# Kernel optimization log

Measured on AMD Instinct MI355X. Metric: run time of the kernel, lower is better.

## Reference

```python
import jax, jax.numpy as jnp
import numpy as np

C = 12        # num_cls
KN = 5        # kernel_num
MU = 2        # kernel_mu
N = 384       # ns == nt (prob_mtx assumes equal sizes)
D = 256       # feature dim


def _cdist(a, b):
    # Euclidean pairwise distance (torch.cdist, p=2)
    d2 = (jnp.sum(a * a, 1)[:, None] + jnp.sum(b * b, 1)[None, :]
          - 2.0 * (a @ b.T))
    return jnp.sqrt(jnp.maximum(d2, 0.0))


def _kern(dist, gamma):
    # dist: (..., N, N) broadcastable against gamma (...,)
    # multi-bandwidth RBF: sum_i exp(-clip(dist / max(gamma*mu^(i-kn//2), 1e-5), 1e-5, 1e5))
    g = gamma[..., None, None]
    acc = 0.0
    for i in range(KN):
        bw = jnp.maximum(g * (MU ** (i - KN // 2)), 1e-5)
        r = jnp.clip(dist / bw, 1e-5, 1e5)
        acc = acc + jnp.exp(-r)
    return acc


def setup_inputs() -> dict:
    key = jax.random.key(0)
    k1, k2, k3, k4 = jax.random.split(key, 4)
    src_x = jax.random.normal(k1, (N, D), dtype=jnp.float32)
    tgt_x = jax.random.normal(k2, (N, D), dtype=jnp.float32)
    src_y = jax.random.randint(k3, (N,), 0, C)
    t = jax.random.uniform(k4, (N, C), dtype=jnp.float32) + 1e-3
    tgt_y = t / t.sum(axis=1, keepdims=True)  # soft pseudo-label probs
    return {"src_x": src_x, "tgt_x": tgt_x, "src_y": src_y, "tgt_y": tgt_y}


def _cdd(src_x, tgt_x, ps, pt):
    E_ss = _cdist(src_x, src_x)
    E_tt = _cdist(tgt_x, tgt_x)
    E_st = _cdist(src_x, tgt_x)

    # per-class weighted distance sums: sum_ij p_i p_j E_ij
    sss = jnp.einsum('ic,ij,jc->c', ps, E_ss, ps)
    stt = jnp.einsum('ic,ij,jc->c', pt, E_tt, pt)
    sst = jnp.einsum('is,ij,jt->st', ps, E_st, pt)
    cs = ps.sum(0)
    ct = pt.sum(0)
    pss = cs * cs          # (C,)  == prob['ss'][c].sum()
    ptt = ct * ct
    pst = cs[:, None] * ct[None, :]  # (C,C)

    # ---------------- intra (diagonal class pairs, src vs tgt) ----------------
    g_in = jax.lax.stop_gradient(
        (sss + stt + 2.0 * jnp.diagonal(sst))
        / (pss + ptt + 2.0 * jnp.diagonal(pst)))   # (C,)

    Pss = ps.T[:, :, None] * ps.T[:, None, :]      # (C,N,N)
    Ptt = pt.T[:, :, None] * pt.T[:, None, :]      # (C,N,N)
    Pst = ps.T[:, :, None] * pt.T[:, None, :]      # (C,N,N) diagonal pairs

    Dss = E_ss[None] * Pss
    Dtt = E_tt[None] * Ptt
    Dst = E_st[None] * Pst

    k1 = (_kern(Dss, g_in) * Pss).sum((-2, -1)) / pss
    k2 = (_kern(Dtt, g_in) * Ptt).sum((-2, -1)) / ptt
    k3 = (_kern(Dst, g_in) * Pst).sum((-2, -1)) / jnp.diagonal(pst)
    intra = (k1 + k2 - 2.0 * k3).sum() / C

    # ---------------- inter (off-diagonal class pairs, src only) --------------
    # edist['ss']==edist['tt']==edist['st']==E_ss; probs from (src_y, src_y)
    sst_s = jnp.einsum('is,ij,jt->st', ps, E_ss, ps)       # (C,C)
    pst_s = cs[:, None] * cs[None, :]
    g2 = jax.lax.stop_gradient(
        (sss[:, None] + sss[None, :] + 2.0 * sst_s)
        / (pss[:, None] + pss[None, :] + 2.0 * pst_s))     # (C,C)

    K1 = _kern(Dss[:, None], g2)                            # (C,C,N,N)
    T1 = jnp.einsum('stij,sij->st', K1, Pss) / pss[:, None]
    K2 = _kern(Dss[None, :], g2)
    T2 = jnp.einsum('stij,tij->st', K2, Pss) / pss[None, :]
    Pst2 = ps.T[:, None, :, None] * ps.T[None, :, None, :]  # (C,C,N,N)
    K3 = _kern(E_ss[None, None] * Pst2, g2)
    T3 = (K3 * Pst2).sum((-2, -1)) / pst_s

    mmd = (T1 + T2 - 2.0 * T3) * (1.0 - jnp.eye(C, dtype=T1.dtype))
    inter = mmd.sum() / (C * C - C)
    return intra, inter


def reference(src_x, tgt_x, src_y, tgt_y):
    ps = jnp.eye(C, dtype=src_x.dtype)[src_y]  # one-hot like torch.eye(num_cls)[src_y]
    return _cdd(src_x, tgt_x, ps, tgt_y)
```

## Files before the change

### kernel.cpp

```cpp
#include <hip/hip_runtime.h>
#include <math.h>

#define NN 147456
#define Nn 384
#define Dd 256
#define Cc 12
#define NTILE 144

__device__ __forceinline__ float kern5(float d, const float* __restrict__ ibw) {
    float acc = 0.f;
#pragma unroll
    for (int k = 0; k < 5; k++) {
        float r = fminf(fmaxf(d * ibw[k], 1e-5f), 1e5f);
        acc += __expf(-r);
    }
    return acc;
}

__device__ __forceinline__ float blockReduceSum(float v, float* sh) {
#pragma unroll
    for (int o = 32; o; o >>= 1) v += __shfl_xor(v, o, 64);
    __syncthreads();
    if ((threadIdx.x & 63) == 0) sh[threadIdx.x >> 6] = v;
    __syncthreads();
    float r = 0.f;
    if (threadIdx.x == 0) {
        int nw = (int)(blockDim.x >> 6);
        for (int w = 0; w < nw; w++) r += sh[w];
    }
    return r;
}

__global__ __launch_bounds__(256) void cdist_stats_kernel(
        const float* __restrict__ sx, const float* __restrict__ tx,
        const int* __restrict__ ys, const float* __restrict__ pt,
        float* __restrict__ Ebase, float* __restrict__ P0T,
        float* __restrict__ P1T, float* __restrict__ P2T,
        float* __restrict__ out) {
    int z = blockIdx.z;
    int tid = threadIdx.x;
    int i0 = blockIdx.y * 32, j0 = blockIdx.x * 32;
    int tileIdx = blockIdx.y * 12 + blockIdx.x;
    if (z == 0 && tileIdx == 0 && tid < 2) out[tid] = 0.f;

    const float* X = (z == 1) ? tx : sx;
    const float* Y = (z == 0) ? sx : tx;
    float* Eo = Ebase + z * NN;

    __shared__ float As[32][33];
    __shared__ float Bs[32][33];
    __shared__ float red[144];
    __shared__ int   ysh[32];
    __shared__ float ptish[384];
    if (tid < 32) ysh[tid] = ys[i0 + tid];
    if (tid < 144) red[tid] = 0.f;
    if (z == 1)
        for (int q = tid; q < 384; q += 256) ptish[q] = pt[i0 * 12 + q];

    int tj = tid & 31, ti = tid >> 5;
    float acc[4] = {0.f, 0.f, 0.f, 0.f};
    for (int kk = 0; kk < Dd; kk += 32) {
#pragma unroll
        for (int p = 0; p < 4; p++) {
            int idx = tid + p * 256;
            int r = idx >> 5, k = idx & 31;
            As[r][k] = X[(i0 + r) * Dd + kk + k];
            Bs[r][k] = Y[(j0 + r) * Dd + kk + k];
        }
        __syncthreads();
#pragma unroll
        for (int m = 0; m < 4; m++) {
            int r = ti + m * 8;
            float a = 0.f;
#pragma unroll
            for (int k = 0; k < 32; k++) {
                float d = As[r][k] - Bs[tj][k];
                a = fmaf(d, d, a);
            }
            acc[m] += a;
        }
        __syncthreads();
    }
    float e[4];
#pragma unroll
    for (int m = 0; m < 4; m++) {
        e[m] = sqrtf(acc[m]);
        Eo[(i0 + ti + m * 8) * Nn + j0 + tj] = e[m];
    }

    if (z == 0) {
        int t = ys[j0 + tj];
#pragma unroll
        for (int m = 0; m < 4; m++)
            atomicAdd(&red[ysh[ti + m * 8] * 12 + t], e[m]);
        __syncthreads();
        if (tid < 144) P0T[tid * NTILE + tileIdx] = red[tid];
    } else {
        const float4* p4 = (const float4*)(pt + (j0 + tj) * 12);
        float4 pa = p4[0], pb = p4[1], pc = p4[2];
        float pv[12] = {pa.x, pa.y, pa.z, pa.w, pb.x, pb.y, pb.z, pb.w,
                        pc.x, pc.y, pc.z, pc.w};
#pragma unroll
        for (int c = 0; c < 12; c++) {
            float a = 0.f;
            if (z == 1) {
#pragma unroll
                for (int m = 0; m < 4; m++)
                    a = fmaf(e[m], ptish[(ti + m * 8) * 12 + c], a);
            } else {
#pragma unroll
                for (int m = 0; m < 4; m++)
                    a += (ysh[ti + m * 8] == c) ? e[m] : 0.f;
            }
            float v = a * pv[c];
#pragma unroll
            for (int o = 32; o; o >>= 1) v += __shfl_xor(v, o, 64);
            if ((tid & 63) == 0) atomicAdd(&red[c], v);
        }
        __syncthreads();
        if (tid < 12) {
            if (z == 1) P1T[tid * NTILE + tileIdx] = red[tid];
            else        P2T[tid * NTILE + tileIdx] = red[tid];
        }
    }
}

__global__ __launch_bounds__(384) void eval_kernel(
        const float* __restrict__ E, const int* __restrict__ ys,
        const float* __restrict__ pt, const float* __restrict__ P0T,
        const float* __restrict__ P1T, const float* __restrict__ P2T,
        float* __restrict__ out) {
    int i = blockIdx.x;
    int j = threadIdx.x;
    int s = ys[i];
    __shared__ float st48[48];
    __shared__ float s_cs[12], s_ct[12];
    __shared__ float sh_ibwin[60];
    __shared__ float sh_ibw2s[60];
    __shared__ float sh_invptt[12];
    __shared__ float sh_invccs[12];
    __shared__ float sh_pti[12];
    __shared__ float red[8];
    if (j >= 64 && j < 76)       s_cs[j - 64] = 0.f;
    else if (j >= 80 && j < 92)  s_ct[j - 80] = 0.f;
    else if (j >= 96 && j < 108) sh_pti[j - 96] = pt[i * 12 + (j - 96)];

    int t = ys[j];
    const float4* p4 = (const float4*)(pt + j * 12);
    float4 pa = p4[0], pb = p4[1], pc = p4[2];
    float ptj[12] = {pa.x, pa.y, pa.z, pa.w, pb.x, pb.y, pb.z, pb.w,
                     pc.x, pc.y, pc.z, pc.w};
    float e_ss = E[i * Nn + j];
    float e_tt = E[NN + i * Nn + j];
    float e_st = E[2 * NN + i * Nn + j];
    __syncthreads();

    atomicAdd(&s_cs[t], 1.f);
#pragma unroll
    for (int c = 0; c < 12; c++) {
        float v = ptj[c];
#pragma unroll
        for (int o = 32; o; o >>= 1) v += __shfl_xor(v, o, 64);
        if ((j & 63) == 0) atomicAdd(&s_ct[c], v);
    }
    {
        int g = j >> 3, k = j & 7;
        const float* src;
        if (g < 12)      src = P0T + (g * 13) * NTILE;
        else if (g < 24) src = P0T + (s * 12 + (g - 12)) * NTILE;
        else if (g < 36) src = P1T + (g - 24) * NTILE;
        else             src = P2T + (g - 36) * NTILE;
        float v = 0.f;
#pragma unroll
        for (int q = 0; q < 18; q++) v += src[k * 18 + q];
#pragma unroll
        for (int o = 1; o < 8; o <<= 1) v += __shfl_xor(v, o, 64);
        if (k == 0) st48[g] = v;
    }
    __syncthreads();
    const float MUP[5] = {0.25f, 0.5f, 1.f, 2.f, 4.f};
    if (j < 12) {
        int c = j;
        float cs = s_cs[c], ct2 = s_ct[c];
        float g = (st48[c] + st48[24 + c] + 2.f * st48[36 + c])
                  / ((cs + ct2) * (cs + ct2));
#pragma unroll
        for (int k = 0; k < 5; k++)
            sh_ibwin[c * 5 + k] = 1.f / fmaxf(g * MUP[k], 1e-5f);
        sh_invptt[c] = 1.f / (ct2 * ct2);
    } else if (j >= 64 && j < 76) {
        int tp = j - 64;
        float css = s_cs[s], cst = s_cs[tp];
        float g2 = (st48[s] + st48[tp] + 2.f * st48[12 + tp])
                   / ((css + cst) * (css + cst));
#pragma unroll
        for (int k = 0; k < 5; k++)
            sh_ibw2s[tp * 5 + k] = 1.f / fmaxf(g2 * MUP[k], 1e-5f);
        sh_invccs[tp] = 1.f / (css * cst);
    }
    __syncthreads();
    float invpss_s = 1.f / (s_cs[s] * s_cs[s]);
    float invcst_s = 1.f / (s_cs[s] * s_ct[s]);

    float si = 0.f, se = 0.f;
#pragma unroll
    for (int c = 0; c < 12; c++) {
        float w = sh_pti[c] * ptj[c];
        si = fmaf(kern5(e_tt * w, &sh_ibwin[c * 5]) * w, sh_invptt[c], si);
    }
    {
        float w = 0.f;
#pragma unroll
        for (int c = 0; c < 12; c++) w = (c == s) ? ptj[c] : w;
        si = fmaf(-2.f * kern5(e_st * w, &sh_ibwin[s * 5]) * w, invcst_s, si);
    }
    if (t == s) {
        si = fmaf(kern5(e_ss, &sh_ibwin[s * 5]), invpss_s, si);
        float ts = -kern5(e_ss, &sh_ibw2s[s * 5]);
#pragma unroll
        for (int tp = 0; tp < 12; tp++)
            ts += kern5(e_ss, &sh_ibw2s[tp * 5]);
        se = fmaf(2.f * ts, invpss_s, se);
    } else {
        se = fmaf(-2.f * kern5(e_ss, &sh_ibw2s[t * 5]), sh_invccs[t], se);
    }
    si = blockReduceSum(si, red);
    se = blockReduceSum(se, red);
    if (j == 0) {
        atomicAdd(&out[0], si * (1.f / 12.f));
        atomicAdd(&out[1], se * (1.f / 132.f));
    }
}

extern "C" void kernel_launch(void* const* d_in, const int* in_sizes, int n_in,
                              void* d_out, int out_size, void* d_ws, size_t ws_size,
                              hipStream_t stream) {
    (void)in_sizes; (void)n_in; (void)out_size; (void)ws_size;
    const float* sx = (const float*)d_in[0];
    const float* tx = (const float*)d_in[1];
    const int*   ys = (const int*)d_in[2];
    const float* pt = (const float*)d_in[3];
    float* out = (float*)d_out;
    float* ws  = (float*)d_ws;
    float* E   = ws;
    float* P0T = ws + 3 * NN;
    float* P1T = P0T + 144 * NTILE;
    float* P2T = P1T + 12 * NTILE;

    cdist_stats_kernel<<<dim3(12, 12, 3), 256, 0, stream>>>(sx, tx, ys, pt,
                                                            E, P0T, P1T, P2T, out);
    eval_kernel<<<384, 384, 0, stream>>>(E, ys, pt, P0T, P1T, P2T, out);
}
```

Before: 48.85 us.

## Compute cdist via norm expansion with full-K smem tile and drop kernel clamps

Result: faster. 40.67 us (-16.7%).

```diff
diff --git a/kernel.cpp b/kernel.cpp
--- a/kernel.cpp
+++ b/kernel.cpp
@@ -6,14 +6,12 @@
 #define Dd 256
 #define Cc 12
 #define NTILE 144
-
-__device__ __forceinline__ float kern5(float d, const float* __restrict__ ibw) {
+#define PADK 260
+
+__device__ __forceinline__ float kern5(float d, const float* __restrict__ nibw) {
     float acc = 0.f;
 #pragma unroll
-    for (int k = 0; k < 5; k++) {
-        float r = fminf(fmaxf(d * ibw[k], 1e-5f), 1e5f);
-        acc += __expf(-r);
-    }
+    for (int k = 0; k < 5; k++) acc += __expf(d * nibw[k]);
     return acc;
 }
 
@@ -31,7 +29,7 @@
     return r;
 }
 
-__global__ __launch_bounds__(256) void cdist_stats_kernel(
+__global__ __launch_bounds__(256, 2) void cdist_stats_kernel(
         const float* __restrict__ sx, const float* __restrict__ tx,
         const int* __restrict__ ys, const float* __restrict__ pt,
         float* __restrict__ Ebase, float* __restrict__ P0T,
@@ -47,44 +45,60 @@
     const float* Y = (z == 0) ? sx : tx;
     float* Eo = Ebase + z * NN;
 
-    __shared__ float As[32][33];
-    __shared__ float Bs[32][33];
+    __shared__ float As[32 * PADK];
+    __shared__ float Bs[32 * PADK];
+    __shared__ float nA[32], nB[32];
     __shared__ float red[144];
     __shared__ int   ysh[32];
     __shared__ float ptish[384];
+
+    {
+        const float4* Xv = (const float4*)(X + i0 * Dd);
+        const float4* Yv = (const float4*)(Y + j0 * Dd);
+#pragma unroll
+        for (int it = 0; it < 8; it++) {
+            int q = tid + it * 256;
+            int r = q >> 6, c = q & 63;
+            *(float4*)&As[r * PADK + c * 4] = Xv[q];
+            *(float4*)&Bs[r * PADK + c * 4] = Yv[q];
+        }
+    }
+    __syncthreads();
+
+    {
+        int n = tid >> 2, qu = tid & 3;
+        const float* src = (n < 32) ? &As[n * PADK] : &Bs[(n - 32) * PADK];
+        float s = 0.f;
+#pragma unroll
+        for (int q = 0; q < 16; q++) {
+            float4 v = *(const float4*)&src[(qu * 16 + q) * 4];
+            s = fmaf(v.x, v.x, fmaf(v.y, v.y, fmaf(v.z, v.z, fmaf(v.w, v.w, s))));
+        }
+        s += __shfl_xor(s, 1, 64);
+        s += __shfl_xor(s, 2, 64);
+        if (qu == 0) { if (n < 32) nA[n] = s; else nB[n - 32] = s; }
+    }
     if (tid < 32) ysh[tid] = ys[i0 + tid];
     if (tid < 144) red[tid] = 0.f;
-    if (z == 1)
-        for (int q = tid; q < 384; q += 256) ptish[q] = pt[i0 * 12 + q];
+    if (z == 1) { ptish[tid] = pt[i0 * 12 + tid]; if (tid < 128) ptish[256 + tid] = pt[i0 * 12 + 256 + tid]; }
+    __syncthreads();
 
     int tj = tid & 31, ti = tid >> 5;
-    float acc[4] = {0.f, 0.f, 0.f, 0.f};
-    for (int kk = 0; kk < Dd; kk += 32) {
-#pragma unroll
-        for (int p = 0; p < 4; p++) {
-            int idx = tid + p * 256;
-            int r = idx >> 5, k = idx & 31;
-            As[r][k] = X[(i0 + r) * Dd + kk + k];
-            Bs[r][k] = Y[(j0 + r) * Dd + kk + k];
-        }
-        __syncthreads();
+    float dot[4] = {0.f, 0.f, 0.f, 0.f};
+#pragma unroll 4
+    for (int q = 0; q < 64; q++) {
+        float4 b = *(const float4*)&Bs[tj * PADK + q * 4];
 #pragma unroll
         for (int m = 0; m < 4; m++) {
-            int r = ti + m * 8;
-            float a = 0.f;
-#pragma unroll
-            for (int k = 0; k < 32; k++) {
-                float d = As[r][k] - Bs[tj][k];
-                a = fmaf(d, d, a);
-            }
-            acc[m] += a;
-        }
-        __syncthreads();
+            float4 a = *(const float4*)&As[(ti + m * 8) * PADK + q * 4];
+            dot[m] = fmaf(a.x, b.x, fmaf(a.y, b.y, fmaf(a.z, b.z, fmaf(a.w, b.w, dot[m]))));
+        }
     }
     float e[4];
 #pragma unroll
     for (int m = 0; m < 4; m++) {
-        e[m] = sqrtf(acc[m]);
+        float d2 = nA[ti + m * 8] + nB[tj] - 2.f * dot[m];
+        e[m] = sqrtf(fmaxf(d2, 0.f));
         Eo[(i0 + ti + m * 8) * Nn + j0 + tj] = e[m];
     }
 
@@ -186,7 +200,7 @@
                   / ((cs + ct2) * (cs + ct2));
 #pragma unroll
         for (int k = 0; k < 5; k++)
-            sh_ibwin[c * 5 + k] = 1.f / fmaxf(g * MUP[k], 1e-5f);
+            sh_ibwin[c * 5 + k] = -1.f / fmaxf(g * MUP[k], 1e-5f);
         sh_invptt[c] = 1.f / (ct2 * ct2);
     } else if (j >= 64 && j < 76) {
         int tp = j - 64;
@@ -195,7 +209,7 @@
                    / ((css + cst) * (css + cst));
 #pragma unroll
         for (int k = 0; k < 5; k++)
-            sh_ibw2s[tp * 5 + k] = 1.f / fmaxf(g2 * MUP[k], 1e-5f);
+            sh_ibw2s[tp * 5 + k] = -1.f / fmaxf(g2 * MUP[k], 1e-5f);
         sh_invccs[tp] = 1.f / (css * cst);
     }
     __syncthreads();
```
